# Kernel optimization log

Measured on AMD Instinct MI355X. Metric: run time of the kernel, lower is better.

The kernel has to match this reference:

```python
import jax, jax.numpy as jnp
import numpy as np

NUM_HEADS = 16

def setup_inputs() -> dict:
    key = jax.random.key(0)
    ks = jax.random.split(key, 6)
    B, S, D = 2, 2048, 1024
    scale = 1.0 / np.sqrt(D)
    x = jax.random.normal(ks[0], (B, S, D), dtype=jnp.float32)
    mask = jnp.tril(jnp.ones((S, S), dtype=jnp.int32))[None, None, :, :]  # causal [1,1,S,S]
    Wq = jax.random.normal(ks[1], (D, D), dtype=jnp.float32) * scale
    Wk = jax.random.normal(ks[2], (D, D), dtype=jnp.float32) * scale
    Wv = jax.random.normal(ks[3], (D, D), dtype=jnp.float32) * scale
    Wo = jax.random.normal(ks[4], (D, D), dtype=jnp.float32) * scale
    z = jnp.zeros((D,), dtype=jnp.float32)
    return {"x": x, "mask": mask, "Wq": Wq, "bq": z, "Wk": Wk, "bk": z,
            "Wv": Wv, "bv": z, "Wo": Wo, "bo": z}

def reference(x, mask, Wq, bq, Wk, bk, Wv, bv, Wo, bo):
    B, S, D = x.shape
    H = NUM_HEADS
    hd = D // H
    # torch Linear: y = x @ W.T + b
    def proj(W, b):
        return (x @ W.T + b).reshape(B, S, H, hd).transpose(0, 2, 1, 3)  # [B,H,S,hd]
    q = proj(Wq, bq)
    k = proj(Wk, bk)
    v = proj(Wv, bv)
    # NOTE: original module does NOT scale by 1/sqrt(d_k) -- faithful to source.
    scores = jnp.einsum('bhqd,bhkd->bhqk', q, k)  # [B,H,S,S]
    scores = jnp.where(mask == 0, jnp.float32(-10000.0), scores)
    attn = jax.nn.softmax(scores, axis=-1)
    # dropout omitted for deterministic reference (eval-mode equivalent)
    out = jnp.einsum('bhqk,bhkd->bhqd', attn, v)
    out = out.transpose(0, 2, 1, 3).reshape(B, S, D)
    return out @ Wo.T + bo
```

## Files before the change

### kernel.cpp

```cpp
#include <hip/hip_runtime.h>

#define S_LEN 2048
#define DM    1024
#define NHEAD 16
#define HDIM  64
#define NB    2
#define NROWS (NB * S_LEN)
#define RCP_LN2 1.44269504f

using f32x4  = __attribute__((ext_vector_type(4))) float;
using f16x8  = __attribute__((ext_vector_type(8))) _Float16;

__device__ __forceinline__ ushort f2h(float f) {
  return __builtin_bit_cast(ushort, (_Float16)f);
}
__device__ __forceinline__ unsigned pkrtz(float a, float b) {
  return __builtin_bit_cast(unsigned, __builtin_amdgcn_cvt_pkrtz(a, b));
}
__device__ __forceinline__ float fexp2(float x) {
  return __builtin_amdgcn_exp2f(x);
}
__device__ __forceinline__ f32x4 mfma16(f16x8 a, f16x8 b, f32x4 c) {
  return __builtin_amdgcn_mfma_f32_16x16x32_f16(a, b, c, 0, 0, 0);
}
__device__ __forceinline__ void async16(const ushort* g, ushort* l) {
  __builtin_amdgcn_global_load_lds(
      (const __attribute__((address_space(1))) unsigned*)g,
      (__attribute__((address_space(3))) unsigned*)l, 16, 0, 0);
}

__device__ const int g_qi_tab[24] = {15,15,7,14,14,13,13,6,12,12,11,11,
                                     5,10,10,9,9,4,8,8,3,2,1,0};
__device__ const int g_hf_tab[24] = {0,1,2,0,1,0,1,2,0,1,0,1,
                                     2,0,1,0,1,2,0,1,2,2,2,2};

__global__ void tohalf5(const float* __restrict__ x,  const float* __restrict__ wq,
                        const float* __restrict__ wk, const float* __restrict__ wv,
                        const float* __restrict__ wo,
                        ushort* __restrict__ Xh, ushort* __restrict__ Wh,
                        ushort* __restrict__ Woh) {
  constexpr int X4 = (NROWS * DM) / 4;
  constexpr int W4 = (DM * DM) / 4;
  const size_t WN = (size_t)DM * DM;
  int i = blockIdx.x * 256 + threadIdx.x;
  const float4* src; ushort4* dst; int k;
  if (i < X4)               { src = (const float4*)x;  dst = (ushort4*)Xh;        k = i; }
  else if (i < X4 + W4)     { src = (const float4*)wq; dst = (ushort4*)Wh;        k = i - X4; }
  else if (i < X4 + 2*W4)   { src = (const float4*)wk; dst = (ushort4*)(Wh+WN);   k = i - X4 - W4; }
  else if (i < X4 + 3*W4)   { src = (const float4*)wv; dst = (ushort4*)(Wh+2*WN); k = i - X4 - 2*W4; }
  else                      { src = (const float4*)wo; dst = (ushort4*)Woh;       k = i - X4 - 3*W4; }
  float4 v = src[k];
  dst[k] = make_ushort4(f2h(v.x), f2h(v.y), f2h(v.z), f2h(v.w));
}

template<int EPI, int MFRAG, int NFRAG>
__global__ __launch_bounds__(256, 2)
void gemm_half(const ushort* __restrict__ A, const ushort* __restrict__ B,
               const float* __restrict__ biasQ, const float* __restrict__ biasK,
               const float* __restrict__ biasV,
               float* __restrict__ outF,
               ushort* __restrict__ Q, ushort* __restrict__ Kd,
               ushort* __restrict__ Vt, int Ncols)
{
  constexpr int KD = 1024;
  constexpr int BM = MFRAG * 32, BN = NFRAG * 32;
  constexpr int NCH = (BM + BN) / 8;
  constexpr int CPW = NCH / 4;
  __shared__ ushort sL[(BM + BN) * 64];
  const int t = threadIdx.x;
  const int w = t >> 6, l = t & 63;
  const int lr = l >> 4, lc = l & 15;
  const int wr = w >> 1, wc = w & 1;
  const int nwg = gridDim.x * gridDim.y;
  const int lin = blockIdx.y * gridDim.x + blockIdx.x;
  const int per8 = nwg >> 3;
  const int swz = (lin & 7) * per8 + (lin >> 3);
  const int i0 = (swz / gridDim.x) * BM, j0 = (swz % gridDim.x) * BN;

  const int srow = l >> 3;
  const int se   = ((l & 7) ^ srow) << 3;

  const ushort* sp[CPW];
#pragma unroll
  for (int ii = 0; ii < CPW; ++ii) {
    const int c = w * CPW + ii;
    sp[ii] = (c < BM / 8)
        ? A + (size_t)(i0 + c * 8 + srow) * KD + se
        : B + (size_t)(j0 + (c - BM / 8) * 8 + srow) * KD + se;
  }

  f32x4 acc[MFRAG][NFRAG] = {};

  for (int k0 = 0; k0 < KD; k0 += 64) {
#pragma unroll
    for (int ii = 0; ii < CPW; ++ii) {
      async16(sp[ii], &sL[(w * CPW + ii) * 512]);
      sp[ii] += 64;
    }
    asm volatile("s_waitcnt vmcnt(0)" ::: "memory");
    __syncthreads();
#pragma unroll
    for (int kk = 0; kk < 2; ++kk) {
      const int cb = (kk * 64 + lr * 16) ^ ((lc & 7) << 4);
      f16x8 a[MFRAG], b[NFRAG];
#pragma unroll
      for (int m = 0; m < MFRAG; ++m)
        a[m] = *(const f16x8*)&sL[(wr * MFRAG * 16 + m * 16 + lc) * 64 + (cb >> 1)];
#pragma unroll
      for (int n = 0; n < NFRAG; ++n)
        b[n] = *(const f16x8*)&sL[BM * 64 + (wc * NFRAG * 16 + n * 16 + lc) * 64 + (cb >> 1)];
#pragma unroll
      for (int m = 0; m < MFRAG; ++m)
#pragma unroll
        for (int n = 0; n < NFRAG; ++n)
          acc[m][n] = mfma16(a[m], b[n], acc[m][n]);
    }
    __syncthreads();
  }

#pragma unroll
  for (int m = 0; m < MFRAG; ++m)
#pragma unroll
    for (int n = 0; n < NFRAG; ++n) {
      const int jbase = j0 + wc * NFRAG * 16 + n * 16;
      const int ibase = i0 + wr * MFRAG * 16 + m * 16 + lr * 4;
      if constexpr (EPI == 0) {
        const int region = jbase >> 10;
        const int jc0 = jbase & 1023;
        const int h = jc0 >> 6, d0 = jc0 & 63;
        const int b = ibase >> 11, s0 = ibase & 2047;
        const size_t bh = (size_t)(b * NHEAD + h);
        if (region == 0) {
          float bb = biasQ[jc0 + lc];
#pragma unroll
          for (int r = 0; r < 4; ++r)
            Q[(bh * S_LEN + s0 + r) * HDIM + d0 + lc] =
                f2h((acc[m][n][r] + bb) * RCP_LN2);
        } else if (region == 1) {
          float bb = biasK[jc0 + lc];
#pragma unroll
          for (int r = 0; r < 4; ++r)
            Kd[(bh * S_LEN + s0 + r) * HDIM + d0 + lc] = f2h(acc[m][n][r] + bb);
        } else {
          float bb = biasV[jc0 + lc];
          ushort4 pv = make_ushort4(f2h(acc[m][n][0] + bb), f2h(acc[m][n][1] + bb),
                                    f2h(acc[m][n][2] + bb), f2h(acc[m][n][3] + bb));
          *(ushort4*)&Vt[(bh * HDIM + d0 + lc) * S_LEN + s0] = pv;
        }
      } else {
#pragma unroll
        for (int r = 0; r < 4; ++r)
          outF[(size_t)(ibase + r) * Ncols + jbase + lc] =
              acc[m][n][r] + biasQ[jbase + lc];
      }
    }
}

__global__ __launch_bounds__(256, 3)
void attn_kernel(const ushort* __restrict__ Qp, const ushort* __restrict__ Kp,
                 const ushort* __restrict__ Vt, ushort* __restrict__ O,
                 float* __restrict__ Pacc, float* __restrict__ Pml)
{
  __shared__ ushort sKV[2][2 * 64 * 64];
  __shared__ ushort Plds[4][2][16][72];
  const int blk = blockIdx.x;
  const int c = blk & 255, s3 = blk >> 8;
  const int rank = (s3 == 0) ? c : ((s3 == 1) ? 511 - c : 512 + c);
  const int ty = rank >> 5, bh = rank & 31;
  const int qi = g_qi_tab[ty], hf = g_hf_tab[ty];
  const int nkt = 2 * qi + 2;
  const int kt0 = (hf == 1) ? (nkt >> 1) : 0;
  const int kt1 = (hf == 0) ? (nkt >> 1) : nkt;

  const int t = threadIdx.x, w = t >> 6, l = t & 63;
  const int g = l >> 4, q = l & 15;
  const size_t base = (size_t)bh * S_LEN * HDIM;
  const int q0w = qi * 128 + w * 32;

  const int srow = l >> 3;
  const int se   = ((l & 7) ^ srow) << 3;

  const int sel = w >> 1;
  const ushort* sp[4];
  const int sadv = (sel == 0) ? 64 * HDIM : 64;
#pragma unroll
  for (int ii = 0; ii < 4; ++ii) {
    const int sub = (w * 4 + ii) & 7;
    sp[ii] = (sel == 0)
        ? Kp + base + (size_t)(kt0 * 64 + sub * 8 + srow) * HDIM + se
        : Vt + ((size_t)bh * HDIM + sub * 8 + srow) * S_LEN + kt0 * 64 + se;
  }

  auto stage = [&](int buf) {
#pragma unroll
    for (int ii = 0; ii < 4; ++ii) {
      const int sub = (w * 4 + ii) & 7;
      async16(sp[ii], &sKV[buf][sel * 4096 + sub * 512]);
      sp[ii] += sadv;
    }
  };

  f16x8 bQ[2][2];
#pragma unroll
  for (int u = 0; u < 2; ++u)
#pragma unroll
    for (int ks = 0; ks < 2; ++ks)
      bQ[u][ks] = *(const f16x8*)(Qp + base +
                  (size_t)(q0w + u * 16 + q) * HDIM + ks * 32 + g * 8);

  f32x4 oacc[2][4] = {};
  float m[2] = {-3e38f, -3e38f}, lsum[2] = {0.f, 0.f};

  stage(0);
  asm volatile("s_waitcnt vmcnt(0)" ::: "memory");
  __syncthreads();
  int cur = 0;

  for (int kt = kt0; kt < kt1; ++kt) {
    if (kt + 1 < kt1) stage(cur ^ 1);

    if (kt * 64 <= q0w + 31) {
      f32x4 s[2][4] = {};
#pragma unroll
      for (int ks = 0; ks < 2; ++ks) {
        const int cb = (((ks * 64 + g * 16) ^ ((q & 7) << 4)) >> 1);
#pragma unroll
        for (int n = 0; n < 4; ++n) {
          f16x8 kf = *(const f16x8*)&sKV[cur][(n * 16 + q) * 64 + cb];
          s[0][n] = mfma16(kf, bQ[0][ks], s[0][n]);
          s[1][n] = mfma16(kf, bQ[1][ks], s[1][n]);
        }
      }
#pragma unroll
      for (int u = 0; u < 2; ++u) {
        if (kt * 64 + 63 > q0w + u * 16) {
          const int qg = q0w + u * 16 + q;
#pragma unroll
          for (int n = 0; n < 4; ++n)
#pragma unroll
            for (int r = 0; r < 4; ++r) {
              int kg = kt * 64 + n * 16 + g * 4 + r;
              if (kg > qg) s[u][n][r] = -1e30f;
            }
        }
      }
      float pm[2];
#pragma unroll
      for (int u = 0; u < 2; ++u) {
        float p = -3e38f;
#pragma unroll
        for (int n = 0; n < 4; ++n)
          p = fmaxf(p, fmaxf(fmaxf(s[u][n][0], s[u][n][1]),
                             fmaxf(s[u][n][2], s[u][n][3])));
        p = fmaxf(p, __shfl_xor(p, 16));
        p = fmaxf(p, __shfl_xor(p, 32));
        pm[u] = p;
      }
#pragma unroll
      for (int u = 0; u < 2; ++u) {
        if (__any(pm[u] > m[u] + 8.0f)) {
          float mnew = fmaxf(m[u], pm[u]);
          float sc = fexp2(m[u] - mnew);
          m[u] = mnew;
          float scr[4];
#pragma unroll
          for (int r = 0; r < 4; ++r) scr[r] = __shfl(sc, g * 4 + r);
#pragma unroll
          for (int dt = 0; dt < 4; ++dt)
#pragma unroll
            for (int r = 0; r < 4; ++r) oacc[u][dt][r] *= scr[r];
          lsum[u] *= sc;
        }
      }
#pragma unroll
      for (int u = 0; u < 2; ++u) {
        float rs = 0.f;
#pragma unroll
        for (int n = 0; n < 4; ++n)
#pragma unroll
          for (int r = 0; r < 4; ++r) {
            float pe = fexp2(s[u][n][r] - m[u]);
            s[u][n][r] = pe;
            rs += pe;
          }
        rs += __shfl_xor(rs, 16);
        rs += __shfl_xor(rs, 32);
        lsum[u] += rs;
      }
#pragma unroll
      for (int u = 0; u < 2; ++u)
#pragma unroll
        for (int n = 0; n < 4; ++n) {
          uint2 pk = make_uint2(pkrtz(s[u][n][0], s[u][n][1]),
                                pkrtz(s[u][n][2], s[u][n][3]));
          *(uint2*)&Plds[w][u][q][n * 16 + g * 4] = pk;
        }
#pragma unroll
      for (int ks = 0; ks < 2; ++ks) {
        const int cb = (((ks * 64 + g * 16) ^ ((q & 7) << 4)) >> 1);
        f16x8 ap0 = *(const f16x8*)&Plds[w][0][q][ks * 32 + g * 8];
        f16x8 ap1 = *(const f16x8*)&Plds[w][1][q][ks * 32 + g * 8];
#pragma unroll
        for (int dt = 0; dt < 4; ++dt) {
          f16x8 bv = *(const f16x8*)&sKV[cur][4096 + (dt * 16 + q) * 64 + cb];
          oacc[0][dt] = mfma16(ap0, bv, oacc[0][dt]);
          oacc[1][dt] = mfma16(ap1, bv, oacc[1][dt]);
        }
      }
    }
    asm volatile("s_waitcnt vmcnt(0)" ::: "memory");
    __syncthreads();
    cur ^= 1;
  }

  if (hf == 2) {
    const int b = bh >> 4, h = bh & 15;
#pragma unroll
    for (int u = 0; u < 2; ++u) {
      float lsr[4];
#pragma unroll
      for (int r = 0; r < 4; ++r)
        lsr[r] = __builtin_amdgcn_rcpf(__shfl(lsum[u], g * 4 + r));
#pragma unroll
      for (int dt = 0; dt < 4; ++dt)
#pragma unroll
        for (int r = 0; r < 4; ++r) {
          int qg = q0w + u * 16 + g * 4 + r;
          O[((size_t)b * S_LEN + qg) * DM + h * HDIM + dt * 16 + q] =
              f2h(oacc[u][dt][r] * lsr[r]);
        }
    }
  } else {
    const int pidx = (bh * 8 + (qi - 8)) * 2 + hf;
    float* po = Pacc + (size_t)pidx * (128 * 64);
#pragma unroll
    for (int u = 0; u < 2; ++u) {
#pragma unroll
      for (int dt = 0; dt < 4; ++dt)
#pragma unroll
        for (int r = 0; r < 4; ++r)
          po[(w * 32 + u * 16 + g * 4 + r) * 64 + dt * 16 + q] = oacc[u][dt][r];
      if (g == 0) {
        Pml[(size_t)pidx * 256 + (w * 32 + u * 16 + q) * 2]     = m[u];
        Pml[(size_t)pidx * 256 + (w * 32 + u * 16 + q) * 2 + 1] = lsum[u];
      }
    }
  }
}

__global__ void combine_kernel(const float* __restrict__ Pacc,
                               const float* __restrict__ Pml,
                               ushort* __restrict__ O)
{
  int gid = blockIdx.x * 256 + threadIdx.x;
  int row = gid >> 6, col = gid & 63;
  int bh = row >> 10;
  int rr = row & 1023;
  int qi = 8 + (rr >> 7), qr = rr & 127;
  int p0 = (bh * 8 + (qi - 8)) * 2;
  float m1 = Pml[(size_t)p0 * 256 + qr * 2];
  float l1 = Pml[(size_t)p0 * 256 + qr * 2 + 1];
  float m2 = Pml[(size_t)(p0 + 1) * 256 + qr * 2];
  float l2 = Pml[(size_t)(p0 + 1) * 256 + qr * 2 + 1];
  float o1 = Pacc[(size_t)p0 * 8192 + qr * 64 + col];
  float o2 = Pacc[(size_t)(p0 + 1) * 8192 + qr * 64 + col];
  float mf = fmaxf(m1, m2);
  float e1 = fexp2(m1 - mf), e2 = fexp2(m2 - mf);
  float o = o1 * e1 + o2 * e2;
  float lden = l1 * e1 + l2 * e2;
  int b = bh >> 4, h = bh & 15;
  O[((size_t)b * S_LEN + qi * 128 + qr) * DM + h * HDIM + col] = f2h(o / lden);
}

extern "C" void kernel_launch(void* const* d_in, const int* in_sizes, int n_in,
                              void* d_out, int out_size, void* d_ws, size_t ws_size,
                              hipStream_t stream)
{
  const float* x  = (const float*)d_in[0];
  const float* Wq = (const float*)d_in[2];
  const float* bq = (const float*)d_in[3];
  const float* Wk = (const float*)d_in[4];
  const float* bk = (const float*)d_in[5];
  const float* Wv = (const float*)d_in[6];
  const float* bv = (const float*)d_in[7];
  const float* Wo = (const float*)d_in[8];
  const float* bo = (const float*)d_in[9];
  float* out = (float*)d_out;

  char* ws = (char*)d_ws;
  size_t off = 0;
  auto alloc = [&](size_t bytes) { char* p = ws + off; off += bytes; return p; };
  const size_t XN = (size_t)NROWS * DM;
  const size_t WN = (size_t)DM * DM;

  ushort* Xh  = (ushort*)alloc(XN * 2);
  ushort* Wh  = (ushort*)alloc(3 * WN * 2);
  ushort* Woh = (ushort*)alloc(WN * 2);
  ushort* Qb  = (ushort*)alloc(XN * 2);
  ushort* Kb  = (ushort*)alloc(XN * 2);
  ushort* Vt  = (ushort*)alloc(XN * 2);
  ushort* Ob  = (ushort*)alloc(XN * 2);
  float*  Pacc = (float*)alloc((size_t)512 * 128 * 64 * 4);
  float*  Pml  = (float*)alloc((size_t)512 * 256 * 4);
  (void)ws_size; (void)in_sizes; (void)n_in; (void)out_size;

  const int total4 = (int)(XN / 4 + 4 * (WN / 4));
  tohalf5<<<total4 / 256, 256, 0, stream>>>(x, Wq, Wk, Wv, Wo, Xh, Wh, Woh);

  gemm_half<0, 4, 4><<<dim3(24, 32), 256, 0, stream>>>(
      Xh, Wh, bq, bk, bv, nullptr, Qb, Kb, Vt, 3072);
  attn_kernel<<<768, 256, 0, stream>>>(Qb, Kb, Vt, Ob, Pacc, Pml);
  combine_kernel<<<8192, 256, 0, stream>>>(Pacc, Pml, Ob);
  gemm_half<1, 2, 4><<<dim3(8, 64), 256, 0, stream>>>(
      Ob, Woh, bo, nullptr, nullptr, out, nullptr, nullptr, nullptr, 1024);
}
```

Measured before the change: 102.6 us.

## Widen attention KV tile to 128 keys and retile output projection GEMM

The attention kernel now stages 128 keys of K and V per loop iteration instead of 64. This doubles the shared-memory tile, halves the number of iterations and barriers, and reuses one smaller P staging buffer per wave across the two halves. The work-split tables and the half-range computation are rebuilt for the coarser tiles, and launch bounds drop from 3 to 2 blocks per CU to fit the larger LDS and register footprint. The output projection GEMM switches to a narrower tile with twice as many column blocks. The trade-off is lower occupancy and more wasted masked work on diagonal tiles, in exchange for less synchronisation overhead per key.

```diff
diff --git a/kernel.cpp b/kernel.cpp
--- a/kernel.cpp
+++ b/kernel.cpp
@@ -29,10 +29,10 @@
       (__attribute__((address_space(3))) unsigned*)l, 16, 0, 0);
 }
 
-__device__ const int g_qi_tab[24] = {15,15,7,14,14,13,13,6,12,12,11,11,
-                                     5,10,10,9,9,4,8,8,3,2,1,0};
-__device__ const int g_hf_tab[24] = {0,1,2,0,1,0,1,2,0,1,0,1,
-                                     2,0,1,0,1,2,0,1,2,2,2,2};
+__device__ const int g_qi_tab[24] = {15,15,14,7, 14,13,13,12,6, 12,11,11,10,5,
+                                     10,9,9,8,4, 8,3, 2, 1, 0};
+__device__ const int g_hf_tab[24] = {0,1,0,2, 1,0,1,0,2, 1,0,1,0,2,
+                                     1,0,1,0,2, 1,2, 2, 2, 2};
 
 __global__ void tohalf5(const float* __restrict__ x,  const float* __restrict__ wq,
                         const float* __restrict__ wk, const float* __restrict__ wv,
@@ -156,21 +156,22 @@
     }
 }
 
-__global__ __launch_bounds__(256, 3)
+__global__ __launch_bounds__(256, 2)
 void attn_kernel(const ushort* __restrict__ Qp, const ushort* __restrict__ Kp,
                  const ushort* __restrict__ Vt, ushort* __restrict__ O,
                  float* __restrict__ Pacc, float* __restrict__ Pml)
 {
-  __shared__ ushort sKV[2][2 * 64 * 64];
-  __shared__ ushort Plds[4][2][16][72];
+  __shared__ ushort sKV[2][16384];
+  __shared__ ushort Plds[4][16][72];
   const int blk = blockIdx.x;
   const int c = blk & 255, s3 = blk >> 8;
   const int rank = (s3 == 0) ? c : ((s3 == 1) ? 511 - c : 512 + c);
   const int ty = rank >> 5, bh = rank & 31;
   const int qi = g_qi_tab[ty], hf = g_hf_tab[ty];
-  const int nkt = 2 * qi + 2;
-  const int kt0 = (hf == 1) ? (nkt >> 1) : 0;
-  const int kt1 = (hf == 0) ? (nkt >> 1) : nkt;
+  const int nkt = qi + 1;
+  const int ktm = (nkt + 1) >> 1;
+  const int kt0 = (hf == 1) ? ktm : 0;
+  const int kt1 = (hf == 0) ? ktm : nkt;
 
   const int t = threadIdx.x, w = t >> 6, l = t & 63;
   const int g = l >> 4, q = l & 15;
@@ -180,22 +181,27 @@
   const int srow = l >> 3;
   const int se   = ((l & 7) ^ srow) << 3;
 
-  const int sel = w >> 1;
-  const ushort* sp[4];
-  const int sadv = (sel == 0) ? 64 * HDIM : 64;
-#pragma unroll
-  for (int ii = 0; ii < 4; ++ii) {
-    const int sub = (w * 4 + ii) & 7;
-    sp[ii] = (sel == 0)
-        ? Kp + base + (size_t)(kt0 * 64 + sub * 8 + srow) * HDIM + se
-        : Vt + ((size_t)bh * HDIM + sub * 8 + srow) * S_LEN + kt0 * 64 + se;
+  const int isK = (w < 2);
+  const ushort* sp[8];
+  int dst[8];
+  const int sadv = isK ? 128 * HDIM : 128;
+#pragma unroll
+  for (int ii = 0; ii < 8; ++ii) {
+    if (isK) {
+      const int cc = w * 8 + ii;
+      sp[ii]  = Kp + base + (size_t)(kt0 * 128 + cc * 8 + srow) * HDIM + se;
+      dst[ii] = cc * 512;
+    } else {
+      const int idx = (w - 2) * 8 + ii;
+      const int dg = idx >> 1, kh = idx & 1;
+      sp[ii]  = Vt + ((size_t)bh * HDIM + dg * 8 + srow) * S_LEN + kt0 * 128 + kh * 64 + se;
+      dst[ii] = 8192 + kh * 4096 + dg * 512;
+    }
   }
-
   auto stage = [&](int buf) {
 #pragma unroll
-    for (int ii = 0; ii < 4; ++ii) {
-      const int sub = (w * 4 + ii) & 7;
-      async16(sp[ii], &sKV[buf][sel * 4096 + sub * 512]);
+    for (int ii = 0; ii < 8; ++ii) {
+      async16(sp[ii], &sKV[buf][dst[ii]]);
       sp[ii] += sadv;
     }
   };
@@ -219,13 +225,13 @@
   for (int kt = kt0; kt < kt1; ++kt) {
     if (kt + 1 < kt1) stage(cur ^ 1);
 
-    if (kt * 64 <= q0w + 31) {
-      f32x4 s[2][4] = {};
+    if (kt * 128 <= q0w + 31) {
+      f32x4 s[2][8] = {};
 #pragma unroll
       for (int ks = 0; ks < 2; ++ks) {
         const int cb = (((ks * 64 + g * 16) ^ ((q & 7) << 4)) >> 1);
 #pragma unroll
-        for (int n = 0; n < 4; ++n) {
+        for (int n = 0; n < 8; ++n) {
           f16x8 kf = *(const f16x8*)&sKV[cur][(n * 16 + q) * 64 + cb];
           s[0][n] = mfma16(kf, bQ[0][ks], s[0][n]);
           s[1][n] = mfma16(kf, bQ[1][ks], s[1][n]);
@@ -233,13 +239,13 @@
       }
 #pragma unroll
       for (int u = 0; u < 2; ++u) {
-        if (kt * 64 + 63 > q0w + u * 16) {
+        if (kt * 128 + 127 > q0w + u * 16) {
           const int qg = q0w + u * 16 + q;
 #pragma unroll
-          for (int n = 0; n < 4; ++n)
+          for (int n = 0; n < 8; ++n)
 #pragma unroll
             for (int r = 0; r < 4; ++r) {
-              int kg = kt * 64 + n * 16 + g * 4 + r;
+              int kg = kt * 128 + n * 16 + g * 4 + r;
               if (kg > qg) s[u][n][r] = -1e30f;
             }
         }
@@ -249,7 +255,7 @@
       for (int u = 0; u < 2; ++u) {
         float p = -3e38f;
 #pragma unroll
-        for (int n = 0; n < 4; ++n)
+        for (int n = 0; n < 8; ++n)
           p = fmaxf(p, fmaxf(fmaxf(s[u][n][0], s[u][n][1]),
                              fmaxf(s[u][n][2], s[u][n][3])));
         p = fmaxf(p, __shfl_xor(p, 16));
@@ -276,7 +282,7 @@
       for (int u = 0; u < 2; ++u) {
         float rs = 0.f;
 #pragma unroll
-        for (int n = 0; n < 4; ++n)
+        for (int n = 0; n < 8; ++n)
 #pragma unroll
           for (int r = 0; r < 4; ++r) {
             float pe = fexp2(s[u][n][r] - m[u]);
@@ -288,23 +294,26 @@
         lsum[u] += rs;
       }
 #pragma unroll
-      for (int u = 0; u < 2; ++u)
-#pragma unroll
-        for (int n = 0; n < 4; ++n) {
-          uint2 pk = make_uint2(pkrtz(s[u][n][0], s[u][n][1]),
-                                pkrtz(s[u][n][2], s[u][n][3]));
-          *(uint2*)&Plds[w][u][q][n * 16 + g * 4] = pk;
-        }
-#pragma unroll
-      for (int ks = 0; ks < 2; ++ks) {
-        const int cb = (((ks * 64 + g * 16) ^ ((q & 7) << 4)) >> 1);
-        f16x8 ap0 = *(const f16x8*)&Plds[w][0][q][ks * 32 + g * 8];
-        f16x8 ap1 = *(const f16x8*)&Plds[w][1][q][ks * 32 + g * 8];
-#pragma unroll
-        for (int dt = 0; dt < 4; ++dt) {
-          f16x8 bv = *(const f16x8*)&sKV[cur][4096 + (dt * 16 + q) * 64 + cb];
-          oacc[0][dt] = mfma16(ap0, bv, oacc[0][dt]);
-          oacc[1][dt] = mfma16(ap1, bv, oacc[1][dt]);
+      for (int h = 0; h < 2; ++h) {
+#pragma unroll
+        for (int u = 0; u < 2; ++u) {
+#pragma unroll
+          for (int np = 0; np < 4; ++np) {
+            const int n = h * 4 + np;
+            uint2 pk = make_uint2(pkrtz(s[u][n][0], s[u][n][1]),
+                                  pkrtz(s[u][n][2], s[u][n][3]));
+            *(uint2*)&Plds[w][q][np * 16 + g * 4] = pk;
+          }
+#pragma unroll
+          for (int ks = 0; ks < 2; ++ks) {
+            f16x8 ap = *(const f16x8*)&Plds[w][q][ks * 32 + g * 8];
+            const int cb = (((ks * 64 + g * 16) ^ ((q & 7) << 4)) >> 1);
+#pragma unroll
+            for (int dt = 0; dt < 4; ++dt) {
+              f16x8 bv = *(const f16x8*)&sKV[cur][8192 + h * 4096 + (dt * 16 + q) * 64 + cb];
+              oacc[u][dt] = mfma16(ap, bv, oacc[u][dt]);
+            }
+          }
         }
       }
     }
@@ -411,6 +420,6 @@
       Xh, Wh, bq, bk, bv, nullptr, Qb, Kb, Vt, 3072);
   attn_kernel<<<768, 256, 0, stream>>>(Qb, Kb, Vt, Ob, Pacc, Pml);
   combine_kernel<<<8192, 256, 0, stream>>>(Pacc, Pml, Ob);
-  gemm_half<1, 2, 4><<<dim3(8, 64), 256, 0, stream>>>(
+  gemm_half<1, 2, 2><<<dim3(16, 64), 256, 0, stream>>>(
       Ob, Woh, bo, nullptr, nullptr, out, nullptr, nullptr, nullptr, 1024);
 }
```

New measurement: 105.3 us. 2.6% more time.
